# Optimization experiments

Hardware: AMD Instinct MI355X
Metric: run time of the kernel (lower is better)

The kernel has to match this reference:

```python
import jax, jax.numpy as jnp
import numpy as np

SR = 22050
FMIN = 220.0
N_BINS = 84
BPO = 12
HOP = 512
NORM_P = 1
T_SAMPLES = 8388608  # 2**23 samples of audio


def _make_kernels():
    Q = 1.0 / (2.0 ** (1.0 / BPO) - 1.0)
    fftLen = 2 ** int(np.ceil(np.log2(np.ceil(Q * SR / FMIN))))  # 2048
    freqs = FMIN * 2.0 ** (np.arange(N_BINS) / float(BPO))
    temp = np.zeros((N_BINS, fftLen), dtype=np.complex64)
    for k in range(N_BINS):
        freq = freqs[k]
        l = np.ceil(Q * SR / freq)
        if l % 2 == 1:
            start = int(np.ceil(fftLen / 2.0 - l / 2.0)) - 1
        else:
            start = int(np.ceil(fftLen / 2.0 - l / 2.0))
        li = int(l)
        n = np.arange(li)
        hann = 0.5 - 0.5 * np.cos(2 * np.pi * n / li)  # periodic ('fftbins=True') hann
        idx = np.arange(np.floor(-l / 2.0), np.floor(l / 2.0))
        temp[k, start:start + li] = hann * np.exp(1j * 2 * np.pi * freq / SR * idx) / li
    spec = np.fft.fft(temp, axis=1)[:, : fftLen // 2 + 1]
    kr = spec.real.astype(np.float32)
    ki = spec.imag.astype(np.float32)
    # norm=1 branch: divide by L1 norm (over bins axis, dim=0) of complex magnitude
    mag = np.sqrt(kr ** 2 + ki ** 2)
    denom = np.sum(np.abs(mag), axis=0)  # shape [freq_bins]
    kr = (kr / denom).astype(np.float32)
    ki = (ki / denom).astype(np.float32)
    # Fourier kernels: freq_scale='no', windowing='no'
    freq_bins = fftLen // 2 + 1
    s = np.arange(fftLen, dtype=np.float64)
    kk = np.arange(freq_bins, dtype=np.float64)
    ang = 2 * np.pi * np.outer(kk, s) / fftLen  # [freq_bins, fftLen]
    wsin = np.sin(ang).astype(np.float32)
    wcos = np.cos(ang).astype(np.float32)
    return kr, ki, wcos, wsin


def setup_inputs() -> dict:
    key = jax.random.key(0)
    x = jax.random.normal(key, (T_SAMPLES,), dtype=jnp.float32)
    kr, ki, wcos, wsin = _make_kernels()
    return {
        "x": x,
        "wcos": jnp.asarray(wcos),
        "wsin": jnp.asarray(wsin),
        "kr": jnp.asarray(kr),
        "ki": jnp.asarray(ki),
    }


def reference(x, wcos, wsin, kr, ki):
    fftLen = wcos.shape[1]  # 2048
    n_frames = (x.shape[0] - fftLen) // HOP + 1  # static under jit
    # frame the signal: equivalent to conv1d(x, w, stride=HOP) with kernels w
    idx = jnp.arange(n_frames)[:, None] * HOP + jnp.arange(fftLen)[None, :]
    frames = x[idx]  # [n_frames, fftLen]
    fourier_real = jnp.einsum("fn,kn->kf", frames, wcos)  # [freq_bins, n_frames]
    fourier_imag = jnp.einsum("fn,kn->kf", frames, wsin)
    cqt_real = kr @ fourier_real - ki @ fourier_imag  # [n_bins, n_frames]
    cqt_imag = kr @ fourier_imag + ki @ fourier_real
    cqt = jnp.sqrt(cqt_real ** 2 + cqt_imag ** 2)
    return cqt[None]  # [1, n_bins, n_frames]
```

## Files before the change

### kernel.cpp

```cpp
#include <hip/hip_runtime.h>


#define HOPS 512
#define NBINS 84
#define FREQB 1025
#define FFTLEN 2048
#define NFRAMES 16381
#define LASTF 16380
#define TSAMP 8388608
#define SPAN 34304
#define XLSZ 34572
#define KP16 138
#define WSLICE 23
#define NSPL 6

typedef short bf16x8 __attribute__((ext_vector_type(8)));
typedef float f32x16 __attribute__((ext_vector_type(16)));

union B8 { struct { ushort4 lo, hi; } p; bf16x8 v; uint4 u; };

__device__ __forceinline__ unsigned short f32_to_bf16(float f) {
    union { float f; unsigned u; } v; v.f = f;
    return (unsigned short)((v.u + 0x7FFFu + ((v.u >> 16) & 1u)) >> 16);
}
__device__ __forceinline__ unsigned pk_bf16(float lo, float hi) {
    return (unsigned)f32_to_bf16(lo) | ((unsigned)f32_to_bf16(hi) << 16);
}
__device__ __forceinline__ bf16x8 pack8(const float* s) {
    B8 r;
    r.u.x = pk_bf16(s[0], s[1]); r.u.y = pk_bf16(s[2], s[3]);
    r.u.z = pk_bf16(s[4], s[5]); r.u.w = pk_bf16(s[6], s[7]);
    return r.v;
}

__global__ __launch_bounds__(64) void aprep_kernel(
    const float* __restrict__ kr, const float* __restrict__ ki,
    unsigned short* __restrict__ Apf)
{
    const int bid = blockIdx.x;
    const int mt = bid / KP16, k16 = bid % KP16;
    const int l = threadIdx.x;
    const int c32 = l & 31, h = l >> 5;
    const int row = mt * 32 + c32;
    const int b = row >> 1, im = row & 1;
    const bool bok = b < NBINS;
    const float* cosp = (im ? ki : kr) + (size_t)(bok ? b : 0) * FREQB;
    const float* sinp = (im ? kr : ki) + (size_t)(bok ? b : 0) * FREQB;
    const float ssign = im ? 1.f : -1.f;

    unsigned short o[8];
    #pragma unroll
    for (int j = 0; j < 8; ++j) {
        int k = k16 * 16 + h * 8 + j;
        float v = 0.f;
        if (bok) {
            if (k <= 1024)       v = cosp[k];
            else if (k <= 2049)  v = ssign * sinp[k - 1025];
        }
        o[j] = f32_to_bf16(v);
    }
    #pragma unroll
    for (int j = 0; j < 8; ++j)
        Apf[(size_t)bid * 512 + l * 8 + j] = o[j];
}

__global__ __launch_bounds__(64) void wgemm_kernel(
    const float* __restrict__ wcos, const float* __restrict__ wsin,
    const unsigned short* __restrict__ Apf, float* __restrict__ Pp)
{
    const int bid = blockIdx.x;
    const int nt = bid & 63;
    const int rest = bid >> 6;
    const int mt = rest % 6, s = rest / 6;
    const int l = threadIdx.x;
    const int c32 = l & 31, h = l >> 5;
    const int n = nt * 32 + c32;

    f32x16 acc;
    #pragma unroll
    for (int i = 0; i < 16; ++i) acc[i] = 0.f;

    const unsigned short* ap = Apf + (size_t)(mt * KP16 + s * WSLICE) * 512 + l * 8;

    for (int i = 0; i < WSLICE; ++i) {
        const int k16 = s * WSLICE + i;
        if (k16 > 128) break;
        B8 af; af.u = *(const uint4*)(ap + (size_t)i * 512);
        float bv[8];
        const int kb = k16 * 16 + h * 8;
        if (k16 <= 63) {
            #pragma unroll
            for (int j = 0; j < 8; ++j)
                bv[j] = wcos[(size_t)(kb + j) * FFTLEN + n];
        } else if (k16 >= 65 && k16 <= 127) {
            const int mb = kb - 1025;
            #pragma unroll
            for (int j = 0; j < 8; ++j)
                bv[j] = wsin[(size_t)(mb + j) * FFTLEN + n];
        } else {
            #pragma unroll
            for (int j = 0; j < 8; ++j) {
                int k = kb + j;
                float t = 0.f;
                if (k <= 1024)      t = wcos[(size_t)k * FFTLEN + n];
                else if (k <= 2049) t = wsin[(size_t)(k - 1025) * FFTLEN + n];
                bv[j] = t;
            }
        }
        acc = __builtin_amdgcn_mfma_f32_32x32x16_bf16(af.v, pack8(bv), acc, 0, 0, 0);
    }

    float* dst = Pp + (size_t)s * (192 * FFTLEN);
    #pragma unroll
    for (int r = 0; r < 16; ++r) {
        int row = mt * 32 + (r & 3) + 8 * (r >> 2) + 4 * h;
        dst[(size_t)row * FFTLEN + n] = acc[r];
    }
}

__global__ __launch_bounds__(256) void combine_kernel(
    const float* __restrict__ Pp, unsigned short* __restrict__ Wpf)
{
    const int gid = blockIdx.x * 256 + threadIdx.x;
    const int mg = gid >> 13;
    const int r = gid & 8191;
    const int k16 = r >> 6, l = r & 63;
    const int c32 = l & 31, h = l >> 5;
    const int row = mg * 32 + c32;
    const int n0 = k16 * 16 + h * 8;

    float4 s0 = make_float4(0.f, 0.f, 0.f, 0.f), s1 = s0;
    const float* base = Pp + (size_t)row * FFTLEN + n0;
    #pragma unroll
    for (int s = 0; s < NSPL; ++s) {
        const float* p = base + (size_t)s * (192 * FFTLEN);
        float4 a = *(const float4*)(p);
        float4 b = *(const float4*)(p + 4);
        s0.x += a.x; s0.y += a.y; s0.z += a.z; s0.w += a.w;
        s1.x += b.x; s1.y += b.y; s1.z += b.z; s1.w += b.w;
    }
    uint4 o;
    o.x = pk_bf16(s0.x, s0.y); o.y = pk_bf16(s0.z, s0.w);
    o.z = pk_bf16(s1.x, s1.y); o.w = pk_bf16(s1.z, s1.w);
    ((uint4*)Wpf)[gid] = o;
}

__global__ __launch_bounds__(768) void cqt_kernel(
    const float* __restrict__ x, const unsigned short* __restrict__ Wpf,
    float* __restrict__ out)
{
    __shared__ __align__(16) unsigned short xl[XLSZ];

    const int t = threadIdx.x;
    const int f0 = blockIdx.x * 64;
    const long S0 = (long)f0 * HOPS;
    const int valid = (int)((TSAMP - S0) < (long)SPAN ? (TSAMP - S0) : (long)SPAN);

    #pragma unroll
    for (int i = 0; i < 12; ++i) {
        int idx4 = t + i * 768;
        if (idx4 < 8576) {
            int s = idx4 * 4;
            float4 v = make_float4(0.f, 0.f, 0.f, 0.f);
            if (s + 4 <= valid) v = *(const float4*)(x + S0 + s);
            ushort4 o;
            o.x = f32_to_bf16(v.x); o.y = f32_to_bf16(v.y);
            o.z = f32_to_bf16(v.z); o.w = f32_to_bf16(v.w);
            *(ushort4*)(&xl[s + 4 * (s >> 9)]) = o;
        }
    }
    __syncthreads();

    const int w = t >> 6, l = t & 63;
    const int mg = w >> 1, fg = w & 1;
    const int c32 = l & 31, h = l >> 5;

    const unsigned short* apf = Wpf + (size_t)mg * (128 * 512) + l * 8;
    const int sbase = (fg * 32 + c32) * HOPS + h * 8;

    f32x16 acc;
    #pragma unroll
    for (int i = 0; i < 16; ++i) acc[i] = 0.f;

    auto ldsB = [&](int k16) -> bf16x8 {
        int s = sbase + k16 * 16;
        int off = s + 4 * (s >> 9);
        B8 r;
        r.p.lo = *(const ushort4*)(&xl[off]);
        r.p.hi = *(const ushort4*)(&xl[off + 4]);
        return r.v;
    };

    uint4 Abuf[2][8];
    #pragma unroll
    for (int j = 0; j < 8; ++j)
        Abuf[0][j] = *(const uint4*)(apf + (size_t)j * 512);

    #pragma unroll
    for (int c = 0; c < 16; ++c) {
        const int cur = c & 1, nxt = cur ^ 1;
        if (c < 15) {
            #pragma unroll
            for (int j = 0; j < 8; ++j)
                Abuf[nxt][j] = *(const uint4*)(apf + (size_t)((c + 1) * 8 + j) * 512);
        }
        #pragma unroll
        for (int j = 0; j < 8; ++j) {
            B8 af; af.u = Abuf[cur][j];
            acc = __builtin_amdgcn_mfma_f32_32x32x16_bf16(af.v, ldsB(c * 8 + j), acc, 0, 0, 0);
        }
    }

    const int f = f0 + fg * 32 + c32;
    if (f < NFRAMES) {
        #pragma unroll
        for (int rp = 0; rp < 4; ++rp) {
            int base = mg * 32 + 8 * rp + 4 * h;
            int b0 = base >> 1;
            float r0 = acc[4 * rp + 0], i0 = acc[4 * rp + 1];
            float r1 = acc[4 * rp + 2], i1 = acc[4 * rp + 3];
            if (b0 < NBINS)
                out[(size_t)b0 * NFRAMES + f] = sqrtf(r0 * r0 + i0 * i0);
            if (b0 + 1 < NBINS)
                out[(size_t)(b0 + 1) * NFRAMES + f] = sqrtf(r1 * r1 + i1 * i1);
        }
    }
}

extern "C" void kernel_launch(void* const* d_in, const int* in_sizes, int n_in,
                              void* d_out, int out_size, void* d_ws, size_t ws_size,
                              hipStream_t stream) {
    const float* x    = (const float*)d_in[0];
    const float* wcos = (const float*)d_in[1];
    const float* wsin = (const float*)d_in[2];
    const float* kr   = (const float*)d_in[3];
    const float* ki   = (const float*)d_in[4];
    float* out = (float*)d_out;

    unsigned short* Wpf = (unsigned short*)d_ws;
    unsigned short* Apf = (unsigned short*)((char*)d_ws + 786432);
    float* Pp = (float*)((char*)d_ws + 786432 + 847872);

    aprep_kernel<<<dim3(6 * KP16), dim3(64), 0, stream>>>(kr, ki, Apf);
    wgemm_kernel<<<dim3(2304), dim3(64), 0, stream>>>(wcos, wsin, Apf, Pp);
    combine_kernel<<<dim3(192), dim3(256), 0, stream>>>(Pp, Wpf);
    cqt_kernel<<<dim3(256), dim3(768), 0, stream>>>(x, Wpf, out);
}
```

Baseline: 128.3 us.

## Halve CQT block waves and compute two frame tiles per wave to reuse A

The CQT kernel now launches 384 threads (6 waves) per block instead of 768. Each wave covers one 32-row output group across both 32-frame tiles, so every A fragment loaded from global memory feeds two MFMAs. This halves global A traffic per block and allows more blocks per CU via launch bounds (384,3). In exchange each wave holds two accumulators and has a rolled double-buffer loop, which raises register pressure and leaves fewer waves to hide latency.

```diff
diff --git a/kernel.cpp b/kernel.cpp
--- a/kernel.cpp
+++ b/kernel.cpp
@@ -6,10 +6,9 @@
 #define FREQB 1025
 #define FFTLEN 2048
 #define NFRAMES 16381
-#define LASTF 16380
 #define TSAMP 8388608
 #define SPAN 34304
-#define XLSZ 34572
+#define XLSZ 34576
 #define KP16 138
 #define WSLICE 23
 #define NSPL 6
@@ -145,7 +144,7 @@
     ((uint4*)Wpf)[gid] = o;
 }
 
-__global__ __launch_bounds__(768) void cqt_kernel(
+__global__ __launch_bounds__(384, 3) void cqt_kernel(
     const float* __restrict__ x, const unsigned short* __restrict__ Wpf,
     float* __restrict__ out)
 {
@@ -156,9 +155,9 @@
     const long S0 = (long)f0 * HOPS;
     const int valid = (int)((TSAMP - S0) < (long)SPAN ? (TSAMP - S0) : (long)SPAN);
 
-    #pragma unroll
-    for (int i = 0; i < 12; ++i) {
-        int idx4 = t + i * 768;
+    #pragma unroll 1
+    for (int i = 0; i < 23; ++i) {
+        int idx4 = t + i * 384;
         if (idx4 < 8576) {
             int s = idx4 * 4;
             float4 v = make_float4(0.f, 0.f, 0.f, 0.f);
@@ -172,17 +171,17 @@
     __syncthreads();
 
     const int w = t >> 6, l = t & 63;
-    const int mg = w >> 1, fg = w & 1;
-    const int c32 = l & 31, h = l >> 5;
-
-    const unsigned short* apf = Wpf + (size_t)mg * (128 * 512) + l * 8;
-    const int sbase = (fg * 32 + c32) * HOPS + h * 8;
-
-    f32x16 acc;
-    #pragma unroll
-    for (int i = 0; i < 16; ++i) acc[i] = 0.f;
-
-    auto ldsB = [&](int k16) -> bf16x8 {
+    const int c32 = l & 31, h = l >> 5;
+
+    const unsigned short* apf = Wpf + (size_t)w * (128 * 512) + l * 8;
+    const int sb0 = c32 * HOPS + h * 8;
+    const int sb1 = (32 + c32) * HOPS + h * 8;
+
+    f32x16 acc0, acc1;
+    #pragma unroll
+    for (int i = 0; i < 16; ++i) { acc0[i] = 0.f; acc1[i] = 0.f; }
+
+    auto ldsB = [&](int sbase, int k16) -> bf16x8 {
         int s = sbase + k16 * 16;
         int off = s + 4 * (s >> 9);
         B8 r;
@@ -191,38 +190,53 @@
         return r.v;
     };
 
-    uint4 Abuf[2][8];
+    uint4 A0[8], A1[8];
     #pragma unroll
     for (int j = 0; j < 8; ++j)
-        Abuf[0][j] = *(const uint4*)(apf + (size_t)j * 512);
-
-    #pragma unroll
-    for (int c = 0; c < 16; ++c) {
-        const int cur = c & 1, nxt = cur ^ 1;
-        if (c < 15) {
-            #pragma unroll
-            for (int j = 0; j < 8; ++j)
-                Abuf[nxt][j] = *(const uint4*)(apf + (size_t)((c + 1) * 8 + j) * 512);
-        }
+        A0[j] = *(const uint4*)(apf + (size_t)j * 512);
+
+    #pragma unroll 1
+    for (int c = 0; c < 16; c += 2) {
+        #pragma unroll
+        for (int j = 0; j < 8; ++j)
+            A1[j] = *(const uint4*)(apf + (size_t)((c + 1) * 8 + j) * 512);
         #pragma unroll
         for (int j = 0; j < 8; ++j) {
-            B8 af; af.u = Abuf[cur][j];
-            acc = __builtin_amdgcn_mfma_f32_32x32x16_bf16(af.v, ldsB(c * 8 + j), acc, 0, 0, 0);
-        }
-    }
-
-    const int f = f0 + fg * 32 + c32;
-    if (f < NFRAMES) {
+            B8 af; af.u = A0[j];
+            int k16 = c * 8 + j;
+            acc0 = __builtin_amdgcn_mfma_f32_32x32x16_bf16(af.v, ldsB(sb0, k16), acc0, 0, 0, 0);
+            acc1 = __builtin_amdgcn_mfma_f32_32x32x16_bf16(af.v, ldsB(sb1, k16), acc1, 0, 0, 0);
+        }
+        if (c + 2 < 16) {
+            #pragma unroll
+            for (int j = 0; j < 8; ++j)
+                A0[j] = *(const uint4*)(apf + (size_t)((c + 2) * 8 + j) * 512);
+        }
         #pragma unroll
-        for (int rp = 0; rp < 4; ++rp) {
-            int base = mg * 32 + 8 * rp + 4 * h;
-            int b0 = base >> 1;
-            float r0 = acc[4 * rp + 0], i0 = acc[4 * rp + 1];
-            float r1 = acc[4 * rp + 2], i1 = acc[4 * rp + 3];
-            if (b0 < NBINS)
-                out[(size_t)b0 * NFRAMES + f] = sqrtf(r0 * r0 + i0 * i0);
-            if (b0 + 1 < NBINS)
-                out[(size_t)(b0 + 1) * NFRAMES + f] = sqrtf(r1 * r1 + i1 * i1);
+        for (int j = 0; j < 8; ++j) {
+            B8 af; af.u = A1[j];
+            int k16 = (c + 1) * 8 + j;
+            acc0 = __builtin_amdgcn_mfma_f32_32x32x16_bf16(af.v, ldsB(sb0, k16), acc0, 0, 0, 0);
+            acc1 = __builtin_amdgcn_mfma_f32_32x32x16_bf16(af.v, ldsB(sb1, k16), acc1, 0, 0, 0);
+        }
+    }
+
+    #pragma unroll
+    for (int nt = 0; nt < 2; ++nt) {
+        const f32x16& acc = nt ? acc1 : acc0;
+        int f = f0 + nt * 32 + c32;
+        if (f < NFRAMES) {
+            #pragma unroll
+            for (int rp = 0; rp < 4; ++rp) {
+                int base = w * 32 + 8 * rp + 4 * h;
+                int b0 = base >> 1;
+                float r0 = acc[4 * rp + 0], i0 = acc[4 * rp + 1];
+                float r1 = acc[4 * rp + 2], i1 = acc[4 * rp + 3];
+                if (b0 < NBINS)
+                    out[(size_t)b0 * NFRAMES + f] = sqrtf(r0 * r0 + i0 * i0);
+                if (b0 + 1 < NBINS)
+                    out[(size_t)(b0 + 1) * NFRAMES + f] = sqrtf(r1 * r1 + i1 * i1);
+            }
         }
     }
 }
@@ -244,5 +258,5 @@
     aprep_kernel<<<dim3(6 * KP16), dim3(64), 0, stream>>>(kr, ki, Apf);
     wgemm_kernel<<<dim3(2304), dim3(64), 0, stream>>>(wcos, wsin, Apf, Pp);
     combine_kernel<<<dim3(192), dim3(256), 0, stream>>>(Pp, Wpf);
-    cqt_kernel<<<dim3(256), dim3(768), 0, stream>>>(x, Wpf, out);
-}
+    cqt_kernel<<<dim3(256), dim3(384), 0, stream>>>(x, Wpf, out);
+}
```

After: 132.8 us. 1.04x slower.
